# Optimization experiments

Measured on AMD Instinct MI355X. Metric: run time of the kernel, lower is better.

Reference implementation:

```python
import jax, jax.numpy as jnp
import numpy as np

IN_F = (16, 16, 16)
OUT_F = (16, 16, 16)
RANKS = (8, 8, 8, 8, 8, 8)


def setup_inputs() -> dict:
    key = jax.random.key(0)
    ks = jax.random.split(key, 9)
    x = jax.random.normal(ks[0], (4096, int(np.prod(IN_F))), dtype=jnp.float32)
    # core ~ U[0,1)*0.1 as in torch.rand(ranks)*0.1
    core = jax.random.uniform(ks[1], RANKS, dtype=jnp.float32) * 0.1
    # factor matrices: 3 out-side (out_f[i], r[i]) then 3 in-side (in_f[i], r[i+3])
    shapes = [(OUT_F[i], RANKS[i]) for i in range(3)] + [(IN_F[i], RANKS[i + 3]) for i in range(3)]
    f0, f1, f2, f3, f4, f5 = [
        jax.random.normal(ks[2 + i], shapes[i], dtype=jnp.float32) * 0.1 for i in range(6)
    ]
    bias = jnp.zeros((int(np.prod(OUT_F)),), dtype=jnp.float32)
    return {"x": x, "core": core, "f0": f0, "f1": f1, "f2": f2,
            "f3": f3, "f4": f4, "f5": f5, "bias": bias}


def reference(x, core, f0, f1, f2, f3, f4, f5, bias):
    # x: [N, prod(IN_F)] -> [N, i1, i2, i3]
    xr = x.reshape(-1, *IN_F)
    # Reconstruct full dense weight from Tucker factors (faithful to original)
    # core: [r0..r5]; f0..f2 out-side (out_dim, r); f3..f5 in-side (in_dim, r)
    W = jnp.einsum('ijklmn,ai,bj,ck,dl,em,fn->abcdef', core, f0, f1, f2, f3, f4, f5)
    # Contract input with in-side modes: [N, o1, o2, o3]
    res = jnp.einsum('abcdef,ndef->nabc', W, xr)
    y = res.reshape(-1, int(np.prod(OUT_F)))
    return y + bias
```

## Files before the change

### kernel.cpp

```cpp
#include <hip/hip_runtime.h>

#define THREADS 256

typedef __attribute__((ext_vector_type(8))) short bf16x8;
typedef __attribute__((ext_vector_type(4))) float f32x4;

__device__ inline unsigned short f2bf(float f) {
    union { float f; unsigned int u; } v; v.f = f;
    unsigned int r = v.u + 0x7fffu + ((v.u >> 16) & 1u);
    return (unsigned short)(r >> 16);
}
__device__ inline unsigned int pack2(float lo, float hi) {
    return (unsigned int)f2bf(lo) | ((unsigned int)f2bf(hi) << 16);
}
__device__ inline float bflo(unsigned int u) {
    union { unsigned int u; float f; } v; v.u = u << 16; return v.f;
}
__device__ inline float bfhi(unsigned int u) {
    union { unsigned int u; float f; } v; v.u = u & 0xffff0000u; return v.f;
}

__global__ __launch_bounds__(THREADS) void k_in_contract2(
    const float* __restrict__ x,
    const float* __restrict__ f3, const float* __restrict__ f4,
    const float* __restrict__ f5, const float* __restrict__ core,
    unsigned short* __restrict__ u3b, unsigned short* __restrict__ coreb,
    int N)
{
    const int n0 = blockIdx.x * 2;
    const int t  = threadIdx.x;

    __shared__ float fs[256];
    __shared__ float u1s[2][256 * 9];
    __shared__ float u2s[2][128 * 9];

    if (t < 128) { fs[t] = f3[t]; fs[128 + t] = f4[t]; }

    if (blockIdx.x < 256) {
        const int i = blockIdx.x * THREADS + t;
        float4 c = ((const float4*)core)[i];
        ushort4 o;
        o.x = f2bf(c.x); o.y = f2bf(c.y); o.z = f2bf(c.z); o.w = f2bf(c.w);
        ((ushort4*)coreb)[i] = o;
    }

    float xv[2][16];
    #pragma unroll
    for (int rr = 0; rr < 2; ++rr) {
        const float4* xr = (const float4*)(x + (size_t)(n0 + rr) * 4096 + t * 16);
        float4 a0 = xr[0], a1 = xr[1], a2 = xr[2], a3 = xr[3];
        xv[rr][0]=a0.x;  xv[rr][1]=a0.y;  xv[rr][2]=a0.z;  xv[rr][3]=a0.w;
        xv[rr][4]=a1.x;  xv[rr][5]=a1.y;  xv[rr][6]=a1.z;  xv[rr][7]=a1.w;
        xv[rr][8]=a2.x;  xv[rr][9]=a2.y;  xv[rr][10]=a2.z; xv[rr][11]=a2.w;
        xv[rr][12]=a3.x; xv[rr][13]=a3.y; xv[rr][14]=a3.z; xv[rr][15]=a3.w;
    }

    float acc8[2][8];
    #pragma unroll
    for (int q = 0; q < 8; ++q) { acc8[0][q] = 0.f; acc8[1][q] = 0.f; }
    #pragma unroll
    for (int f = 0; f < 16; ++f) {
        #pragma unroll
        for (int n6 = 0; n6 < 8; ++n6) {
            const float w = f5[f*8 + n6];
            acc8[0][n6] = fmaf(xv[0][f], w, acc8[0][n6]);
            acc8[1][n6] = fmaf(xv[1][f], w, acc8[1][n6]);
        }
    }
    __syncthreads();
    #pragma unroll
    for (int n6 = 0; n6 < 8; ++n6) {
        u1s[0][t*9 + n6] = acc8[0][n6];
        u1s[1][t*9 + n6] = acc8[1][n6];
    }
    __syncthreads();

    {
        const int d = t >> 4, m = (t >> 1) & 7, h = t & 1;
        float fr[16];
        #pragma unroll
        for (int e = 0; e < 16; ++e) fr[e] = fs[128 + e*8 + m];
        float a4[2][4] = {};
        #pragma unroll
        for (int e = 0; e < 16; ++e) {
            const int base = (d*16 + e)*9 + h*4;
            #pragma unroll
            for (int q = 0; q < 4; ++q) {
                a4[0][q] = fmaf(u1s[0][base + q], fr[e], a4[0][q]);
                a4[1][q] = fmaf(u1s[1][base + q], fr[e], a4[1][q]);
            }
        }
        #pragma unroll
        for (int q = 0; q < 4; ++q) {
            u2s[0][(d*8 + m)*9 + h*4 + q] = a4[0][q];
            u2s[1][(d*8 + m)*9 + h*4 + q] = a4[1][q];
        }
    }
    __syncthreads();

    {
        const int l = t >> 5, m = (t >> 2) & 7, h = t & 3;
        float fr[16];
        #pragma unroll
        for (int d = 0; d < 16; ++d) fr[d] = fs[d*8 + l];
        float a2[2][2] = {};
        #pragma unroll
        for (int d = 0; d < 16; ++d) {
            const int base = (d*8 + m)*9 + h*2;
            a2[0][0] = fmaf(u2s[0][base],     fr[d], a2[0][0]);
            a2[0][1] = fmaf(u2s[0][base + 1], fr[d], a2[0][1]);
            a2[1][0] = fmaf(u2s[1][base],     fr[d], a2[1][0]);
            a2[1][1] = fmaf(u2s[1][base + 1], fr[d], a2[1][1]);
        }
        ((unsigned int*)u3b)[(size_t)(n0+0) * 256 + t] = pack2(a2[0][0], a2[0][1]);
        ((unsigned int*)u3b)[(size_t)(n0+1) * 256 + t] = pack2(a2[1][0], a2[1][1]);
    }
}

__global__ __launch_bounds__(THREADS) void k_gemm_expand(
    const unsigned short* __restrict__ u3b,
    const unsigned short* __restrict__ coreb,
    const float* __restrict__ f0, const float* __restrict__ f1,
    const float* __restrict__ f2, const float* __restrict__ bias,
    float* __restrict__ y, int N)
{
    __shared__ float        vsS[8 * 520];
    __shared__ unsigned int w1S[8 * 528];
    __shared__ unsigned int w2S[8 * 1300];
    __shared__ float        fsS[256];

    const int t  = threadIdx.x;
    const int r0 = blockIdx.x * 8;

    fsS[t] = (t < 128) ? f0[t] : f1[t - 128];

    {
        const int lane = t & 63, w = t >> 6;
        const int lr = lane & 15, lq = lane >> 4;
        const unsigned short* ap = u3b + (size_t)(r0 + (lr & 7)) * 512 + lq * 8;
        const unsigned short* bp = coreb + (size_t)(w * 128 + lr) * 512 + lq * 8;

        f32x4 acc[8];
        #pragma unroll
        for (int c = 0; c < 8; ++c) acc[c] = (f32x4){0.f, 0.f, 0.f, 0.f};

        #pragma unroll
        for (int k0 = 0; k0 < 512; k0 += 32) {
            bf16x8 a = *(const bf16x8*)(ap + k0);
            #pragma unroll
            for (int c = 0; c < 8; ++c) {
                bf16x8 b = *(const bf16x8*)(bp + c * 8192 + k0);
                acc[c] = __builtin_amdgcn_mfma_f32_16x16x32_bf16(a, b, acc[c], 0, 0, 0);
            }
        }
        if (lq < 2) {
            #pragma unroll
            for (int c = 0; c < 8; ++c)
                #pragma unroll
                for (int q = 0; q < 4; ++q)
                    vsS[(lq*4 + q)*520 + w*128 + c*16 + lr] = acc[c][q];
        }
    }
    __syncthreads();

    {
        const int r = t >> 5, a = (t >> 1) & 15, h = t & 1;
        const float* vrow = vsS + r*520 + h*32;
        float fa[8];
        #pragma unroll
        for (int i = 0; i < 8; ++i) fa[i] = fsS[a*8 + i];
        #pragma unroll
        for (int q2 = 0; q2 < 16; ++q2) {
            float s0 = 0.f, s1 = 0.f;
            #pragma unroll
            for (int i = 0; i < 8; ++i) {
                s0 = fmaf(fa[i], vrow[i*64 + 2*q2],     s0);
                s1 = fmaf(fa[i], vrow[i*64 + 2*q2 + 1], s1);
            }
            w1S[r*528 + a*33 + h*16 + q2] = pack2(s0, s1);
        }
    }
    __syncthreads();

    {
        const int r = t >> 5, a = (t >> 1) & 15, h = t & 1;
        const unsigned int* w1row = w1S + r*528 + a*33;
        float acc[8][8] = {};
        #pragma unroll
        for (int j = 0; j < 8; ++j) {
            float wj[8];
            #pragma unroll
            for (int k2 = 0; k2 < 4; ++k2) {
                const unsigned int u = w1row[j*4 + k2];
                wj[2*k2]     = bflo(u);
                wj[2*k2 + 1] = bfhi(u);
            }
            #pragma unroll
            for (int bi = 0; bi < 8; ++bi) {
                const float fb = fsS[128 + (h*8 + bi)*8 + j];
                #pragma unroll
                for (int k = 0; k < 8; ++k)
                    acc[bi][k] = fmaf(fb, wj[k], acc[bi][k]);
            }
        }
        #pragma unroll
        for (int bi = 0; bi < 8; ++bi) {
            const int b = h*8 + bi;
            #pragma unroll
            for (int k2 = 0; k2 < 4; ++k2)
                w2S[r*1300 + a*5 + b*81 + k2] = pack2(acc[bi][2*k2], acc[bi][2*k2+1]);
        }
    }
    __syncthreads();

    {
        const int cq = t & 3, s = t >> 2;
        float f2r[4][8];
        #pragma unroll
        for (int cc = 0; cc < 4; ++cc)
            #pragma unroll
            for (int k = 0; k < 8; ++k)
                f2r[cc][k] = f2[(cq*4 + cc)*8 + k];
        float4 br[4];
        #pragma unroll
        for (int g = 0; g < 4; ++g)
            br[g] = *(const float4*)(bias + (size_t)(s + 64*g)*16 + cq*4);

        #pragma unroll
        for (int r = 0; r < 8; ++r) {
            float4* orow = (float4*)(y + (size_t)(r0 + r) * 4096);
            #pragma unroll
            for (int g = 0; g < 4; ++g) {
                const int ab = s + 64*g, a = ab >> 4, b = ab & 15;
                const unsigned int* w2row = w2S + r*1300 + a*5 + b*81;
                float wf[8];
                #pragma unroll
                for (int k2 = 0; k2 < 4; ++k2) {
                    const unsigned int u = w2row[k2];
                    wf[2*k2]     = bflo(u);
                    wf[2*k2 + 1] = bfhi(u);
                }
                float4 o = br[g];
                #pragma unroll
                for (int k = 0; k < 8; ++k) {
                    o.x = fmaf(f2r[0][k], wf[k], o.x);
                    o.y = fmaf(f2r[1][k], wf[k], o.y);
                    o.z = fmaf(f2r[2][k], wf[k], o.z);
                    o.w = fmaf(f2r[3][k], wf[k], o.w);
                }
                orow[t + 256*g] = o;
            }
        }
    }
}

extern "C" void kernel_launch(void* const* d_in, const int* in_sizes, int n_in,
                              void* d_out, int out_size, void* d_ws, size_t ws_size,
                              hipStream_t stream)
{
    const float* x    = (const float*)d_in[0];
    const float* core = (const float*)d_in[1];
    const float* f0   = (const float*)d_in[2];
    const float* f1   = (const float*)d_in[3];
    const float* f2   = (const float*)d_in[4];
    const float* f3   = (const float*)d_in[5];
    const float* f4   = (const float*)d_in[6];
    const float* f5   = (const float*)d_in[7];
    const float* bias = (const float*)d_in[8];
    float* y = (float*)d_out;

    const int N = in_sizes[0] / 4096;

    unsigned short* u3b   = (unsigned short*)d_ws;
    unsigned short* coreb = u3b + (size_t)N * 512;

    k_in_contract2<<<N / 2, THREADS, 0, stream>>>(x, f3, f4, f5, core, u3b, coreb, N);
    k_gemm_expand<<<N / 8, THREADS, 0, stream>>>(u3b, coreb, f0, f1, f2, bias, y, N);
}
```

Measured before the change: 166.7 us.

## Split Tucker pipeline into six kernels with a standalone tiled MFMA GEMM

Breaks the two fused kernels into separate stages: core conversion, the f5 contraction, the f4/f3 contraction, a 2D-tiled MFMA GEMM against the core, the f0/f1 expansion, and the f2 expansion with bias. Intermediates go to global workspace, with bf16 packing for u1 and w2. The aim is better operand reuse and occupancy in the GEMM than the old per-8-row tiling, which re-read the whole core matrix in every block. In exchange it adds roughly 80 MB of extra global traffic, an fp32 v buffer, and four more kernel launches.

```diff
diff --git a/kernel.cpp b/kernel.cpp
--- a/kernel.cpp
+++ b/kernel.cpp
@@ -20,12 +20,42 @@
     union { unsigned int u; float f; } v; v.u = u & 0xffff0000u; return v.f;
 }
 
-__global__ __launch_bounds__(THREADS) void k_in_contract2(
-    const float* __restrict__ x,
+__global__ __launch_bounds__(THREADS) void k_convert_core(
+    const float* __restrict__ core, unsigned short* __restrict__ coreb)
+{
+    const int i = blockIdx.x * THREADS + threadIdx.x;
+    float4 c = ((const float4*)core)[i];
+    ushort4 o;
+    o.x = f2bf(c.x); o.y = f2bf(c.y); o.z = f2bf(c.z); o.w = f2bf(c.w);
+    ((ushort4*)coreb)[i] = o;
+}
+
+__global__ __launch_bounds__(THREADS) void k_a1(
+    const float* __restrict__ x, const float* __restrict__ f5,
+    uint4* __restrict__ u1b)
+{
+    const int n = blockIdx.x, t = threadIdx.x;
+    const float4* xr = (const float4*)(x + (size_t)n * 4096 + t * 16);
+    float4 a0 = xr[0], a1 = xr[1], a2 = xr[2], a3 = xr[3];
+    float xv[16] = {a0.x,a0.y,a0.z,a0.w, a1.x,a1.y,a1.z,a1.w,
+                    a2.x,a2.y,a2.z,a2.w, a3.x,a3.y,a3.z,a3.w};
+    float acc[8] = {0.f,0.f,0.f,0.f,0.f,0.f,0.f,0.f};
+    #pragma unroll
+    for (int f = 0; f < 16; ++f) {
+        #pragma unroll
+        for (int q = 0; q < 8; ++q)
+            acc[q] = fmaf(xv[f], f5[f*8 + q], acc[q]);
+    }
+    uint4 o;
+    o.x = pack2(acc[0], acc[1]); o.y = pack2(acc[2], acc[3]);
+    o.z = pack2(acc[4], acc[5]); o.w = pack2(acc[6], acc[7]);
+    u1b[(size_t)n * 256 + t] = o;
+}
+
+__global__ __launch_bounds__(THREADS) void k_a23(
+    const uint4* __restrict__ u1b,
     const float* __restrict__ f3, const float* __restrict__ f4,
-    const float* __restrict__ f5, const float* __restrict__ core,
-    unsigned short* __restrict__ u3b, unsigned short* __restrict__ coreb,
-    int N)
+    unsigned short* __restrict__ u3b)
 {
     const int n0 = blockIdx.x * 2;
     const int t  = threadIdx.x;
@@ -36,42 +66,13 @@
 
     if (t < 128) { fs[t] = f3[t]; fs[128 + t] = f4[t]; }
 
-    if (blockIdx.x < 256) {
-        const int i = blockIdx.x * THREADS + t;
-        float4 c = ((const float4*)core)[i];
-        ushort4 o;
-        o.x = f2bf(c.x); o.y = f2bf(c.y); o.z = f2bf(c.z); o.w = f2bf(c.w);
-        ((ushort4*)coreb)[i] = o;
-    }
-
-    float xv[2][16];
     #pragma unroll
     for (int rr = 0; rr < 2; ++rr) {
-        const float4* xr = (const float4*)(x + (size_t)(n0 + rr) * 4096 + t * 16);
-        float4 a0 = xr[0], a1 = xr[1], a2 = xr[2], a3 = xr[3];
-        xv[rr][0]=a0.x;  xv[rr][1]=a0.y;  xv[rr][2]=a0.z;  xv[rr][3]=a0.w;
-        xv[rr][4]=a1.x;  xv[rr][5]=a1.y;  xv[rr][6]=a1.z;  xv[rr][7]=a1.w;
-        xv[rr][8]=a2.x;  xv[rr][9]=a2.y;  xv[rr][10]=a2.z; xv[rr][11]=a2.w;
-        xv[rr][12]=a3.x; xv[rr][13]=a3.y; xv[rr][14]=a3.z; xv[rr][15]=a3.w;
-    }
-
-    float acc8[2][8];
-    #pragma unroll
-    for (int q = 0; q < 8; ++q) { acc8[0][q] = 0.f; acc8[1][q] = 0.f; }
-    #pragma unroll
-    for (int f = 0; f < 16; ++f) {
-        #pragma unroll
-        for (int n6 = 0; n6 < 8; ++n6) {
-            const float w = f5[f*8 + n6];
-            acc8[0][n6] = fmaf(xv[0][f], w, acc8[0][n6]);
-            acc8[1][n6] = fmaf(xv[1][f], w, acc8[1][n6]);
-        }
-    }
-    __syncthreads();
-    #pragma unroll
-    for (int n6 = 0; n6 < 8; ++n6) {
-        u1s[0][t*9 + n6] = acc8[0][n6];
-        u1s[1][t*9 + n6] = acc8[1][n6];
+        uint4 p = u1b[(size_t)(n0 + rr) * 256 + t];
+        u1s[rr][t*9 + 0] = bflo(p.x); u1s[rr][t*9 + 1] = bfhi(p.x);
+        u1s[rr][t*9 + 2] = bflo(p.y); u1s[rr][t*9 + 3] = bfhi(p.y);
+        u1s[rr][t*9 + 4] = bflo(p.z); u1s[rr][t*9 + 5] = bfhi(p.z);
+        u1s[rr][t*9 + 6] = bflo(p.w); u1s[rr][t*9 + 7] = bfhi(p.w);
     }
     __syncthreads();
 
@@ -117,140 +118,123 @@
     }
 }
 
-__global__ __launch_bounds__(THREADS) void k_gemm_expand(
+__global__ __launch_bounds__(THREADS) void k_b(
     const unsigned short* __restrict__ u3b,
     const unsigned short* __restrict__ coreb,
+    float* __restrict__ v)
+{
+    const int t = threadIdx.x, lane = t & 63, w = t >> 6;
+    const int m0 = blockIdx.x * 64 + (w >> 1) * 32;
+    const int p0 = blockIdx.y * 32 + (w & 1) * 16;
+    const int lr = lane & 15, lq = lane >> 4;
+
+    const unsigned short* ap0 = u3b + (size_t)(m0 + lr) * 512 + lq * 8;
+    const unsigned short* ap1 = ap0 + 16 * 512;
+    const unsigned short* bp  = coreb + (size_t)(p0 + lr) * 512 + lq * 8;
+
+    f32x4 acc0 = {0.f,0.f,0.f,0.f}, acc1 = {0.f,0.f,0.f,0.f};
+    #pragma unroll
+    for (int k0 = 0; k0 < 512; k0 += 32) {
+        bf16x8 a0 = *(const bf16x8*)(ap0 + k0);
+        bf16x8 a1 = *(const bf16x8*)(ap1 + k0);
+        bf16x8 b  = *(const bf16x8*)(bp  + k0);
+        acc0 = __builtin_amdgcn_mfma_f32_16x16x32_bf16(a0, b, acc0, 0, 0, 0);
+        acc1 = __builtin_amdgcn_mfma_f32_16x16x32_bf16(a1, b, acc1, 0, 0, 0);
+    }
+    const int col = p0 + lr, row = m0 + lq * 4;
+    #pragma unroll
+    for (int q = 0; q < 4; ++q) {
+        v[(size_t)(row + q) * 512 + col]      = acc0[q];
+        v[(size_t)(row + 16 + q) * 512 + col] = acc1[q];
+    }
+}
+
+__global__ __launch_bounds__(THREADS) void k_c12(
+    const float* __restrict__ v,
     const float* __restrict__ f0, const float* __restrict__ f1,
-    const float* __restrict__ f2, const float* __restrict__ bias,
-    float* __restrict__ y, int N)
-{
-    __shared__ float        vsS[8 * 520];
-    __shared__ unsigned int w1S[8 * 528];
-    __shared__ unsigned int w2S[8 * 1300];
-    __shared__ float        fsS[256];
-
-    const int t  = threadIdx.x;
-    const int r0 = blockIdx.x * 8;
-
-    fsS[t] = (t < 128) ? f0[t] : f1[t - 128];
-
-    {
-        const int lane = t & 63, w = t >> 6;
-        const int lr = lane & 15, lq = lane >> 4;
-        const unsigned short* ap = u3b + (size_t)(r0 + (lr & 7)) * 512 + lq * 8;
-        const unsigned short* bp = coreb + (size_t)(w * 128 + lr) * 512 + lq * 8;
-
-        f32x4 acc[8];
-        #pragma unroll
-        for (int c = 0; c < 8; ++c) acc[c] = (f32x4){0.f, 0.f, 0.f, 0.f};
-
-        #pragma unroll
-        for (int k0 = 0; k0 < 512; k0 += 32) {
-            bf16x8 a = *(const bf16x8*)(ap + k0);
+    uint4* __restrict__ w2b)
+{
+    const int n = blockIdx.x, t = threadIdx.x;
+    __shared__ float fs[256];
+    __shared__ float vs[512];
+    __shared__ float w1s[128 * 9];
+
+    if (t < 128) {
+        fs[t] = f0[t]; fs[128 + t] = f1[t];
+        ((float4*)vs)[t] = ((const float4*)(v + (size_t)n * 512))[t];
+    }
+    __syncthreads();
+
+    {
+        const int a = t >> 4, j = (t >> 1) & 7, h = t & 1;
+        float fa[8];
+        #pragma unroll
+        for (int i = 0; i < 8; ++i) fa[i] = fs[a*8 + i];
+        float a4[4] = {0.f, 0.f, 0.f, 0.f};
+        #pragma unroll
+        for (int i = 0; i < 8; ++i) {
+            const int base = i*64 + j*8 + h*4;
             #pragma unroll
-            for (int c = 0; c < 8; ++c) {
-                bf16x8 b = *(const bf16x8*)(bp + c * 8192 + k0);
-                acc[c] = __builtin_amdgcn_mfma_f32_16x16x32_bf16(a, b, acc[c], 0, 0, 0);
-            }
-        }
-        if (lq < 2) {
-            #pragma unroll
-            for (int c = 0; c < 8; ++c)
-                #pragma unroll
-                for (int q = 0; q < 4; ++q)
-                    vsS[(lq*4 + q)*520 + w*128 + c*16 + lr] = acc[c][q];
-        }
-    }
-    __syncthreads();
-
-    {
-        const int r = t >> 5, a = (t >> 1) & 15, h = t & 1;
-        const float* vrow = vsS + r*520 + h*32;
-        float fa[8];
-        #pragma unroll
-        for (int i = 0; i < 8; ++i) fa[i] = fsS[a*8 + i];
-        #pragma unroll
-        for (int q2 = 0; q2 < 16; ++q2) {
-            float s0 = 0.f, s1 = 0.f;
-            #pragma unroll
-            for (int i = 0; i < 8; ++i) {
-                s0 = fmaf(fa[i], vrow[i*64 + 2*q2],     s0);
-                s1 = fmaf(fa[i], vrow[i*64 + 2*q2 + 1], s1);
-            }
-            w1S[r*528 + a*33 + h*16 + q2] = pack2(s0, s1);
-        }
-    }
-    __syncthreads();
-
-    {
-        const int r = t >> 5, a = (t >> 1) & 15, h = t & 1;
-        const unsigned int* w1row = w1S + r*528 + a*33;
-        float acc[8][8] = {};
+            for (int q = 0; q < 4; ++q)
+                a4[q] = fmaf(vs[base + q], fa[i], a4[q]);
+        }
+        #pragma unroll
+        for (int q = 0; q < 4; ++q) w1s[(a*8 + j)*9 + h*4 + q] = a4[q];
+    }
+    __syncthreads();
+
+    {
+        const int a = t >> 4, b = t & 15;
+        float fb[8];
+        #pragma unroll
+        for (int j = 0; j < 8; ++j) fb[j] = fs[128 + b*8 + j];
+        float a8[8] = {0.f,0.f,0.f,0.f,0.f,0.f,0.f,0.f};
         #pragma unroll
         for (int j = 0; j < 8; ++j) {
-            float wj[8];
-            #pragma unroll
-            for (int k2 = 0; k2 < 4; ++k2) {
-                const unsigned int u = w1row[j*4 + k2];
-                wj[2*k2]     = bflo(u);
-                wj[2*k2 + 1] = bfhi(u);
-            }
-            #pragma unroll
-            for (int bi = 0; bi < 8; ++bi) {
-                const float fb = fsS[128 + (h*8 + bi)*8 + j];
-                #pragma unroll
-                for (int k = 0; k < 8; ++k)
-                    acc[bi][k] = fmaf(fb, wj[k], acc[bi][k]);
-            }
-        }
-        #pragma unroll
-        for (int bi = 0; bi < 8; ++bi) {
-            const int b = h*8 + bi;
-            #pragma unroll
-            for (int k2 = 0; k2 < 4; ++k2)
-                w2S[r*1300 + a*5 + b*81 + k2] = pack2(acc[bi][2*k2], acc[bi][2*k2+1]);
-        }
-    }
-    __syncthreads();
-
-    {
-        const int cq = t & 3, s = t >> 2;
-        float f2r[4][8];
-        #pragma unroll
-        for (int cc = 0; cc < 4; ++cc)
+            const int base = (a*8 + j)*9;
             #pragma unroll
             for (int k = 0; k < 8; ++k)
-                f2r[cc][k] = f2[(cq*4 + cc)*8 + k];
-        float4 br[4];
-        #pragma unroll
-        for (int g = 0; g < 4; ++g)
-            br[g] = *(const float4*)(bias + (size_t)(s + 64*g)*16 + cq*4);
-
-        #pragma unroll
-        for (int r = 0; r < 8; ++r) {
-            float4* orow = (float4*)(y + (size_t)(r0 + r) * 4096);
-            #pragma unroll
-            for (int g = 0; g < 4; ++g) {
-                const int ab = s + 64*g, a = ab >> 4, b = ab & 15;
-                const unsigned int* w2row = w2S + r*1300 + a*5 + b*81;
-                float wf[8];
-                #pragma unroll
-                for (int k2 = 0; k2 < 4; ++k2) {
-                    const unsigned int u = w2row[k2];
-                    wf[2*k2]     = bflo(u);
-                    wf[2*k2 + 1] = bfhi(u);
-                }
-                float4 o = br[g];
-                #pragma unroll
-                for (int k = 0; k < 8; ++k) {
-                    o.x = fmaf(f2r[0][k], wf[k], o.x);
-                    o.y = fmaf(f2r[1][k], wf[k], o.y);
-                    o.z = fmaf(f2r[2][k], wf[k], o.z);
-                    o.w = fmaf(f2r[3][k], wf[k], o.w);
-                }
-                orow[t + 256*g] = o;
-            }
-        }
+                a8[k] = fmaf(w1s[base + k], fb[j], a8[k]);
+        }
+        uint4 o;
+        o.x = pack2(a8[0], a8[1]); o.y = pack2(a8[2], a8[3]);
+        o.z = pack2(a8[4], a8[5]); o.w = pack2(a8[6], a8[7]);
+        w2b[(size_t)n * 256 + t] = o;
+    }
+}
+
+__global__ __launch_bounds__(THREADS) void k_c3(
+    const uint4* __restrict__ w2b, const float* __restrict__ f2,
+    const float* __restrict__ bias, float* __restrict__ y)
+{
+    const int n = blockIdx.x, t = threadIdx.x, cq = t & 3;
+    __shared__ float f2s[128];
+    if (t < 128) f2s[t] = f2[t];
+    __syncthreads();
+
+    float f2r[4][8];
+    #pragma unroll
+    for (int cc = 0; cc < 4; ++cc)
+        #pragma unroll
+        for (int k = 0; k < 8; ++k)
+            f2r[cc][k] = f2s[(cq*4 + cc)*8 + k];
+
+    float4* orow = (float4*)(y + (size_t)n * 4096);
+    #pragma unroll
+    for (int g = 0; g < 4; ++g) {
+        const int ab = (t >> 2) + 64 * g;
+        uint4 p = w2b[(size_t)n * 256 + ab];
+        float wf[8] = {bflo(p.x), bfhi(p.x), bflo(p.y), bfhi(p.y),
+                       bflo(p.z), bfhi(p.z), bflo(p.w), bfhi(p.w)};
+        float4 o = *(const float4*)(bias + ab*16 + cq*4);
+        #pragma unroll
+        for (int k = 0; k < 8; ++k) {
+            o.x = fmaf(f2r[0][k], wf[k], o.x);
+            o.y = fmaf(f2r[1][k], wf[k], o.y);
+            o.z = fmaf(f2r[2][k], wf[k], o.z);
+            o.w = fmaf(f2r[3][k], wf[k], o.w);
+        }
+        orow[t + 256 * g] = o;
     }
 }
 
@@ -271,9 +255,18 @@
 
     const int N = in_sizes[0] / 4096;
 
-    unsigned short* u3b   = (unsigned short*)d_ws;
-    unsigned short* coreb = u3b + (size_t)N * 512;
-
-    k_in_contract2<<<N / 2, THREADS, 0, stream>>>(x, f3, f4, f5, core, u3b, coreb, N);
-    k_gemm_expand<<<N / 8, THREADS, 0, stream>>>(u3b, coreb, f0, f1, f2, bias, y, N);
-}
+    char* p = (char*)d_ws;
+    uint4*          u1b   = (uint4*)p;                 p += (size_t)N * 256 * 16;
+    uint4*          w2b   = (uint4*)p;                 p += (size_t)N * 256 * 16;
+    float*          v     = (float*)p;                 p += (size_t)N * 512 * 4;
+    unsigned short* u3b   = (unsigned short*)p;        p += (size_t)N * 512 * 2;
+    unsigned short* coreb = (unsigned short*)p;
+
+    k_convert_core<<<256, THREADS, 0, stream>>>(core, coreb);
+    k_a1 <<<N, THREADS, 0, stream>>>(x, f5, u1b);
+    k_a23<<<N / 2, THREADS, 0, stream>>>(u1b, f3, f4, u3b);
+    dim3 gb(N / 64, 16);
+    k_b  <<<gb, THREADS, 0, stream>>>(u3b, coreb, v);
+    k_c12<<<N, THREADS, 0, stream>>>(v, f0, f1, w2b);
+    k_c3 <<<N, THREADS, 0, stream>>>(w2b, f2, bias, y);
+}
```

Result: slower. 178.5 us (+7.1%).
